# Performance work log

Measured on AMD Instinct MI355X. Metric: run time of the kernel, lower is better.

## Reference

```python
import jax, jax.numpy as jnp
import numpy as np

N_QUBITS = 6      # 4 data + 2 ancilla
N_DATA = 4
N_LAYERS = 4
N_GROUPS = 8
DIM = 2 ** N_QUBITS  # 64 statevector amplitudes (real: RY + CNOT keep state real)
GN_GROUPS = 32
EPS = 1e-5


def _cnot_ring_perm():
    # CNOT(q, q+1 mod n) ring applied sequentially; compose into one basis permutation.
    n = N_QUBITS
    f = np.arange(DIM)
    for c in range(n):
        t = (c + 1) % n
        cbit = (f >> (n - 1 - c)) & 1
        f = np.where(cbit == 1, f ^ (1 << (n - 1 - t)), f)
    # new_state[f[i]] = old_state[i]  =>  new = old[finv]
    finv = np.empty(DIM, dtype=np.int64)
    finv[f] = np.arange(DIM)
    return jnp.asarray(finv)


def _zsign():
    i = np.arange(DIM)[:, None]
    q = np.arange(N_DATA)[None, :]
    return jnp.asarray(1.0 - 2.0 * ((i >> (N_QUBITS - 1 - q)) & 1), dtype=jnp.float32)


PERM = _cnot_ring_perm()
ZSIGN = _zsign()


def _group_norm(x, gamma, beta):
    B, C, H, W = x.shape
    xg = x.reshape(B, GN_GROUPS, C // GN_GROUPS, H, W)
    mu = xg.mean(axis=(2, 3, 4), keepdims=True)
    var = xg.var(axis=(2, 3, 4), keepdims=True)
    xn = ((xg - mu) * jax.lax.rsqrt(var + EPS)).reshape(B, C, H, W)
    return xn * gamma[None, :, None, None] + beta[None, :, None, None]


def _apply_ry(state, half_angle, q):
    # state: [B,H,W,G,64]; half_angle: [B,H,W,G]; RY = [[c,-s],[s,c]] on qubit q
    pre, post = 2 ** q, 2 ** (N_QUBITS - 1 - q)
    s = state.reshape(state.shape[:-1] + (pre, 2, post))
    c = jnp.cos(half_angle)[..., None, None]
    sn = jnp.sin(half_angle)[..., None, None]
    a0, a1 = s[..., 0, :], s[..., 1, :]
    new = jnp.stack([c * a0 - sn * a1, sn * a0 + c * a1], axis=-2)
    return new.reshape(state.shape)


def _forward(x, emb, gamma, beta, w_in, b_in, theta, w_style, b_style, w_out, b_out):
    B, C, H, W = x.shape
    h = _group_norm(x, gamma, beta)                       # norm0
    emb_a = emb * jax.nn.sigmoid(emb)                     # SiLU(emb)
    # 1x1 projection to per-group data-qubit rotation angles: [B,H,W,G,4]
    ang = jnp.einsum('oc,bchw->bohw', w_in, h) + b_in[None, :, None, None]
    ang = ang.reshape(B, N_GROUPS, N_DATA, H, W).transpose(0, 3, 4, 1, 2)
    # style modulation of circuit parameters: [B,G,L,Q]
    style = (emb_a @ w_style.T + b_style).reshape(B, N_GROUPS, N_LAYERS, N_QUBITS)
    # init |0...0> per pixel per group
    state = jnp.zeros((B, H, W, N_GROUPS, DIM), x.dtype).at[..., 0].set(1.0)
    for l in range(N_LAYERS):
        for q in range(N_QUBITS):
            a = theta[:, l, q][None, None, None, :] + style[:, :, l, q][:, None, None, :]
            if q < N_DATA:                                # data reuploading each layer
                a = a + ang[..., q]
            state = _apply_ry(state, 0.5 * a, q)
        state = state[..., PERM]                          # CNOT ring entangler
    probs = state * state
    meas = probs @ ZSIGN                                  # [B,H,W,G,4] <Z> on data qubits
    meas = meas.transpose(0, 3, 4, 1, 2).reshape(B, N_GROUPS * N_DATA, H, W)
    out = jnp.einsum('oc,bchw->bohw', w_out, meas) + b_out[None, :, None, None]
    return out + x                                        # residual


def setup_inputs() -> dict:
    key = jax.random.key(0)
    ks = jax.random.split(key, 6)
    B, C, H, W, E = 16, 256, 32, 32, 512
    return {
        'x': jax.random.normal(ks[0], (B, C, H, W), jnp.float32),
        'emb': jax.random.normal(ks[1], (B, E), jnp.float32),
        'gamma': jnp.ones((C,), jnp.float32),
        'beta': jnp.zeros((C,), jnp.float32),
        'w_in': jax.random.normal(ks[2], (32, C), jnp.float32) * 0.1,
        'b_in': jnp.zeros((32,), jnp.float32),
        'theta': jax.random.normal(ks[3], (N_GROUPS, N_LAYERS, N_QUBITS), jnp.float32) * 0.5,
        'w_style': jax.random.normal(ks[4], (N_GROUPS * N_LAYERS * N_QUBITS, E), jnp.float32) * 0.02,
        'b_style': jnp.zeros((N_GROUPS * N_LAYERS * N_QUBITS,), jnp.float32),
        'w_out': jax.random.normal(ks[5], (C, 32), jnp.float32) * 0.05,
        'b_out': jnp.zeros((C,), jnp.float32),
    }


def reference(x, emb, gamma, beta, w_in, b_in, theta, w_style, b_style, w_out, b_out):
    return _forward(x, emb, gamma, beta, w_in, b_in, theta, w_style, b_style, w_out, b_out)
```

## Files before the change

kernel.cpp:

```cpp
#include <hip/hip_runtime.h>
#include <math.h>

#define NB 16
#define NC 256
#define NHW 1024
#define NE 512
#define NDQ 4
#define NLQ 4
#define NQB 6
#define QDIM 64
#define PIX 16
#define XPAD 260
#define MSP 20

typedef float v2f __attribute__((ext_vector_type(2)));

struct PermT { int v[QDIM]; };
constexpr PermT make_perm() {
    PermT P{};
    int f[QDIM] = {};
    for (int i = 0; i < QDIM; ++i) f[i] = i;
    for (int c = 0; c < NQB; ++c) {
        int t = (c + 1) % NQB;
        for (int i = 0; i < QDIM; ++i)
            if ((f[i] >> (NQB - 1 - c)) & 1) f[i] ^= 1 << (NQB - 1 - t);
    }
    for (int i = 0; i < QDIM; ++i) P.v[f[i]] = i;
    return P;
}
constexpr PermT PERM = make_perm();

#define ELEM(arr, j) (((j) & 1) ? arr[(j) >> 1].y : arr[(j) >> 1].x)

__global__ __launch_bounds__(256) void k_pre(const float* __restrict__ x,
                                             const float* __restrict__ emb,
                                             const float* __restrict__ w_style,
                                             const float* __restrict__ b_style,
                                             const float* __restrict__ theta,
                                             float* __restrict__ mu,
                                             float* __restrict__ rs,
                                             float* __restrict__ A) {
    if (blockIdx.x < 512) {
        int bg = blockIdx.x;
        const float4* xp = (const float4*)(x + (size_t)bg * 8 * NHW);
        float s = 0.f, ss = 0.f;
        for (int i = threadIdx.x; i < 8 * NHW / 4; i += 256) {
            float4 v = xp[i];
            s  += v.x + v.y + v.z + v.w;
            ss += v.x*v.x + v.y*v.y + v.z*v.z + v.w*v.w;
        }
        __shared__ float red0[4], red1[4];
        #pragma unroll
        for (int o = 32; o; o >>= 1) { s += __shfl_down(s, o); ss += __shfl_down(ss, o); }
        int lane = threadIdx.x & 63, w = threadIdx.x >> 6;
        if (lane == 0) { red0[w] = s; red1[w] = ss; }
        __syncthreads();
        if (threadIdx.x == 0) {
            s  = red0[0] + red0[1] + red0[2] + red0[3];
            ss = red1[0] + red1[1] + red1[2] + red1[3];
            float m = s * (1.f / 8192.f);
            float var = ss * (1.f / 8192.f) - m * m;
            mu[bg] = m;
            rs[bg] = rsqrtf(var + 1e-5f);
        }
    } else {
        int b = blockIdx.x - 512;
        __shared__ float es[NE];
        int t = threadIdx.x;
        for (int i = t; i < NE; i += 256) {
            float v = emb[b * NE + i];
            es[i] = v / (1.f + __expf(-v));
        }
        __syncthreads();
        int j0 = t >> 3, sub = t & 7;
        for (int pass = 0; pass < 6; ++pass) {
            int j = pass * 32 + j0;
            const float* wr = w_style + (size_t)j * NE + sub * 64;
            const float* er = es + sub * 64;
            float acc = 0.f;
            #pragma unroll
            for (int i = 0; i < 64; i += 4) {
                float4 w4 = *(const float4*)(wr + i);
                acc = fmaf(w4.x, er[i],   acc);
                acc = fmaf(w4.y, er[i+1], acc);
                acc = fmaf(w4.z, er[i+2], acc);
                acc = fmaf(w4.w, er[i+3], acc);
            }
            acc += __shfl_xor(acc, 1);
            acc += __shfl_xor(acc, 2);
            acc += __shfl_xor(acc, 4);
            if (sub == 0) A[b * 192 + j] = theta[j] + b_style[j] + acc;
        }
    }
}

__global__ __launch_bounds__(256, 4) void k_main(
    const float* __restrict__ x,
    const float* __restrict__ gamma,
    const float* __restrict__ beta,
    const float* __restrict__ w_in,
    const float* __restrict__ b_in,
    const float* __restrict__ A,
    const float* __restrict__ w_out,
    const float* __restrict__ b_out,
    const float* __restrict__ mu,
    const float* __restrict__ rs,
    float* __restrict__ out) {

    __shared__ float xs[PIX * XPAD];
    __shared__ float as_[PIX * 36];
    __shared__ float ms[32 * MSP];
    __shared__ float scs[NC], shs[NC];

    int blk = blockIdx.x;
    int b = blk >> 6;
    int pbase = (blk & 63) * PIX;
    int t = threadIdx.x;
    int c0 = t >> 2, f4 = (t & 3) * 4;

    float4 xr[4];
    #pragma unroll
    for (int k = 0; k < 4; ++k) {
        int c = c0 + 64 * k;
        xr[k] = *(const float4*)(x + (size_t)(b * NC + c) * NHW + pbase + f4);
    }
    {
        int g = b * 32 + (t >> 3);
        float r = rs[g], m = mu[g];
        float sc = r * gamma[t];
        scs[t] = sc;
        shs[t] = fmaf(-m, sc, beta[t]);
    }
    __syncthreads();

    #pragma unroll
    for (int k = 0; k < 4; ++k) {
        int c = c0 + 64 * k;
        float sc = scs[c], sh = shs[c];
        float4 v = xr[k];
        xs[(f4 + 0) * XPAD + c] = fmaf(v.x, sc, sh);
        xs[(f4 + 1) * XPAD + c] = fmaf(v.y, sc, sh);
        xs[(f4 + 2) * XPAD + c] = fmaf(v.z, sc, sh);
        xs[(f4 + 3) * XPAD + c] = fmaf(v.w, sc, sh);
    }
    __syncthreads();

    {
        int og2 = t >> 4, p = t & 15;
        int o0 = 2 * og2;
        const float* w0r = w_in + o0 * NC;
        const float* w1r = w_in + (o0 + 1) * NC;
        const float* hrow = xs + p * XPAD;
        float a0 = 0.f, a1 = 0.f;
        #pragma unroll 8
        for (int c = 0; c < NC; c += 4) {
            float4 h = *(const float4*)(hrow + c);
            float4 w0 = *(const float4*)(w0r + c);
            float4 w1 = *(const float4*)(w1r + c);
            a0 = fmaf(w0.x, h.x, fmaf(w0.y, h.y, fmaf(w0.z, h.z, fmaf(w0.w, h.w, a0))));
            a1 = fmaf(w1.x, h.x, fmaf(w1.y, h.y, fmaf(w1.z, h.z, fmaf(w1.w, h.w, a1))));
        }
        as_[p * 36 + o0]     = a0 + b_in[o0];
        as_[p * 36 + o0 + 1] = a1 + b_in[o0 + 1];
    }
    __syncthreads();

    #pragma unroll
    for (int k = 0; k < 4; ++k) {
        int c = c0 + 64 * k;
        float4 v = xr[k];
        xs[(f4 + 0) * XPAD + c] = v.x;
        xs[(f4 + 1) * XPAD + c] = v.y;
        xs[(f4 + 2) * XPAD + c] = v.z;
        xs[(f4 + 3) * XPAD + c] = v.w;
    }

    if (t < 128) {
        int g = t >> 4, p = t & 15;
        float4 angv = *(const float4*)(as_ + p * 36 + g * 4);
        float angp[NDQ] = {angv.x, angv.y, angv.z, angv.w};
        float Ar[24];
        {
            const float4* Ab4 = (const float4*)(A + b * 192 + g * 24);
            #pragma unroll
            for (int j = 0; j < 6; ++j) {
                float4 a4 = Ab4[j];
                Ar[4*j] = a4.x; Ar[4*j+1] = a4.y; Ar[4*j+2] = a4.z; Ar[4*j+3] = a4.w;
            }
        }

        v2f st2[QDIM / 2];
        #pragma unroll
        for (int k = 0; k < QDIM / 2; ++k) st2[k] = (v2f){0.f, 0.f};
        st2[0].x = 1.f;

        #pragma unroll
        for (int l = 0; l < NLQ; ++l) {
            #pragma unroll
            for (int q = 0; q < NQB; ++q) {
                float a = Ar[l * NQB + q] + (q < NDQ ? angp[q] : 0.f);
                float sn, cs;
                __sincosf(0.5f * a, &sn, &cs);
                v2f cs2 = {cs, cs};
                if (q < 5) {
                    const int m = 32 >> q;
                    v2f sn2 = {sn, sn};
                    #pragma unroll
                    for (int i = 0; i < QDIM; i += 2) {
                        if (i & m) continue;
                        int klo = i >> 1, khi = (i | m) >> 1;
                        v2f lo = st2[klo], hi = st2[khi];
                        v2f tm = sn2 * hi;
                        v2f um = cs2 * hi;
                        st2[klo] = __builtin_elementwise_fma(cs2, lo, -tm);
                        st2[khi] = __builtin_elementwise_fma(sn2, lo, um);
                    }
                } else {
                    v2f msn = {-sn, sn};
                    #pragma unroll
                    for (int k = 0; k < QDIM / 2; ++k) {
                        v2f a0 = st2[k];
                        v2f asw = __builtin_shufflevector(a0, a0, 1, 0);
                        st2[k] = __builtin_elementwise_fma(msn, asw, cs2 * a0);
                    }
                }
            }
            v2f nst[QDIM / 2];
            #pragma unroll
            for (int k = 0; k < QDIM / 2; ++k) {
                v2f n;
                n.x = ELEM(st2, PERM.v[2 * k]);
                n.y = ELEM(st2, PERM.v[2 * k + 1]);
                nst[k] = n;
            }
            #pragma unroll
            for (int k = 0; k < QDIM / 2; ++k) st2[k] = nst[k];
        }

        float s4[16];
        #pragma unroll
        for (int h = 0; h < 16; ++h) {
            v2f p0 = st2[2 * h] * st2[2 * h];
            v2f p1 = st2[2 * h + 1] * st2[2 * h + 1];
            s4[h] = (p0.x + p0.y) + (p1.x + p1.y);
        }
        float meas[NDQ] = {0.f, 0.f, 0.f, 0.f};
        #pragma unroll
        for (int h = 0; h < 16; ++h) {
            #pragma unroll
            for (int d = 0; d < NDQ; ++d) {
                if ((h >> (3 - d)) & 1) meas[d] -= s4[h];
                else                    meas[d] += s4[h];
            }
        }
        #pragma unroll
        for (int d = 0; d < NDQ; ++d) ms[(g * 4 + d) * MSP + p] = meas[d];
    }
    __syncthreads();

    {
        int c2 = t >> 3, f2 = (t & 7) * 2;
        v2f mreg[32];
        #pragma unroll
        for (int o = 0; o < 32; ++o)
            mreg[o] = *(const v2f*)(ms + o * MSP + f2);
        #pragma unroll
        for (int k = 0; k < 8; ++k) {
            int c = c2 + 32 * k;
            const float* wr = w_out + c * 32;
            float ax = 0.f, ay = 0.f;
            #pragma unroll
            for (int o = 0; o < 32; o += 4) {
                float4 w4 = *(const float4*)(wr + o);
                v2f m0 = mreg[o], m1 = mreg[o+1], m2 = mreg[o+2], m3 = mreg[o+3];
                ax = fmaf(w4.x, m0.x, fmaf(w4.y, m1.x, fmaf(w4.z, m2.x, fmaf(w4.w, m3.x, ax))));
                ay = fmaf(w4.x, m0.y, fmaf(w4.y, m1.y, fmaf(w4.z, m2.y, fmaf(w4.w, m3.y, ay))));
            }
            float bo = b_out[c];
            float x0 = xs[(f2 + 0) * XPAD + c];
            float x1 = xs[(f2 + 1) * XPAD + c];
            float2 r = {ax + bo + x0, ay + bo + x1};
            *(float2*)(out + (size_t)(b * NC + c) * NHW + pbase + f2) = r;
        }
    }
}

extern "C" void kernel_launch(void* const* d_in, const int* in_sizes, int n_in,
                              void* d_out, int out_size, void* d_ws, size_t ws_size,
                              hipStream_t stream) {
    const float* x       = (const float*)d_in[0];
    const float* emb     = (const float*)d_in[1];
    const float* gamma   = (const float*)d_in[2];
    const float* beta    = (const float*)d_in[3];
    const float* w_in    = (const float*)d_in[4];
    const float* b_in    = (const float*)d_in[5];
    const float* theta   = (const float*)d_in[6];
    const float* w_style = (const float*)d_in[7];
    const float* b_style = (const float*)d_in[8];
    const float* w_out   = (const float*)d_in[9];
    const float* b_out   = (const float*)d_in[10];
    float* out = (float*)d_out;

    float* ws = (float*)d_ws;
    float* mu = ws;
    float* rs = ws + 512;
    float* A  = ws + 1024;

    k_pre<<<512 + NB, 256, 0, stream>>>(x, emb, w_style, b_style, theta, mu, rs, A);
    k_main<<<NB * 64, 256, 0, stream>>>(x, gamma, beta, w_in, b_in, A,
                                        w_out, b_out, mu, rs, out);
}
```

Measured before the change: 138.5 us.

## Fuse GroupNorm stats and style projection into main kernel with per-batch spin barrier

Removes the separate pre-pass kernel. Each main block now accumulates GroupNorm sums from the x tile it already loads, and computes part of the style projection, both through global atomics. The 64 blocks of a batch then synchronise on a global counter, with a timeout fallback that recomputes the stats locally. This avoids a second full read of x and one kernel launch, at the cost of a memset, atomics, and a spin barrier that assumes all 64 blocks of a batch are co-resident. With a grid of 1024 blocks at 4 blocks per CU, co-residency should hold on this GPU.

```diff
diff --git a/kernel.cpp b/kernel.cpp
--- a/kernel.cpp
+++ b/kernel.cpp
@@ -32,91 +32,43 @@
 
 #define ELEM(arr, j) (((j) & 1) ? arr[(j) >> 1].y : arr[(j) >> 1].x)
 
-__global__ __launch_bounds__(256) void k_pre(const float* __restrict__ x,
-                                             const float* __restrict__ emb,
-                                             const float* __restrict__ w_style,
-                                             const float* __restrict__ b_style,
-                                             const float* __restrict__ theta,
-                                             float* __restrict__ mu,
-                                             float* __restrict__ rs,
-                                             float* __restrict__ A) {
-    if (blockIdx.x < 512) {
-        int bg = blockIdx.x;
-        const float4* xp = (const float4*)(x + (size_t)bg * 8 * NHW);
-        float s = 0.f, ss = 0.f;
-        for (int i = threadIdx.x; i < 8 * NHW / 4; i += 256) {
-            float4 v = xp[i];
-            s  += v.x + v.y + v.z + v.w;
-            ss += v.x*v.x + v.y*v.y + v.z*v.z + v.w*v.w;
-        }
-        __shared__ float red0[4], red1[4];
-        #pragma unroll
-        for (int o = 32; o; o >>= 1) { s += __shfl_down(s, o); ss += __shfl_down(ss, o); }
-        int lane = threadIdx.x & 63, w = threadIdx.x >> 6;
-        if (lane == 0) { red0[w] = s; red1[w] = ss; }
-        __syncthreads();
-        if (threadIdx.x == 0) {
-            s  = red0[0] + red0[1] + red0[2] + red0[3];
-            ss = red1[0] + red1[1] + red1[2] + red1[3];
-            float m = s * (1.f / 8192.f);
-            float var = ss * (1.f / 8192.f) - m * m;
-            mu[bg] = m;
-            rs[bg] = rsqrtf(var + 1e-5f);
-        }
-    } else {
-        int b = blockIdx.x - 512;
-        __shared__ float es[NE];
-        int t = threadIdx.x;
-        for (int i = t; i < NE; i += 256) {
-            float v = emb[b * NE + i];
-            es[i] = v / (1.f + __expf(-v));
-        }
-        __syncthreads();
-        int j0 = t >> 3, sub = t & 7;
-        for (int pass = 0; pass < 6; ++pass) {
-            int j = pass * 32 + j0;
-            const float* wr = w_style + (size_t)j * NE + sub * 64;
-            const float* er = es + sub * 64;
-            float acc = 0.f;
-            #pragma unroll
-            for (int i = 0; i < 64; i += 4) {
-                float4 w4 = *(const float4*)(wr + i);
-                acc = fmaf(w4.x, er[i],   acc);
-                acc = fmaf(w4.y, er[i+1], acc);
-                acc = fmaf(w4.z, er[i+2], acc);
-                acc = fmaf(w4.w, er[i+3], acc);
-            }
-            acc += __shfl_xor(acc, 1);
-            acc += __shfl_xor(acc, 2);
-            acc += __shfl_xor(acc, 4);
-            if (sub == 0) A[b * 192 + j] = theta[j] + b_style[j] + acc;
-        }
-    }
-}
-
-__global__ __launch_bounds__(256, 4) void k_main(
+#define WS_DONE 1024
+#define WS_A    1056
+#define WS_ZERO_BYTES ((WS_A + 192 * NB) * 4)
+
+__global__ __launch_bounds__(256, 4) void k_mega(
     const float* __restrict__ x,
+    const float* __restrict__ emb,
     const float* __restrict__ gamma,
     const float* __restrict__ beta,
     const float* __restrict__ w_in,
     const float* __restrict__ b_in,
-    const float* __restrict__ A,
+    const float* __restrict__ theta,
+    const float* __restrict__ w_style,
+    const float* __restrict__ b_style,
     const float* __restrict__ w_out,
     const float* __restrict__ b_out,
-    const float* __restrict__ mu,
-    const float* __restrict__ rs,
+    float* __restrict__ ws,
     float* __restrict__ out) {
 
     __shared__ float xs[PIX * XPAD];
     __shared__ float as_[PIX * 36];
     __shared__ float ms[32 * MSP];
-    __shared__ float scs[NC], shs[NC];
+    __shared__ float mure[32], rsre[32];
+    __shared__ float Als[192];
+    __shared__ int s_timeout;
+
+    float* stats_s  = ws;
+    float* stats_ss = ws + 512;
+    unsigned* doneu = (unsigned*)(ws + WS_DONE);
+    float* Ag       = ws + WS_A;
 
     int blk = blockIdx.x;
     int b = blk >> 6;
     int pbase = (blk & 63) * PIX;
     int t = threadIdx.x;
     int c0 = t >> 2, f4 = (t & 3) * 4;
+    int wv = t >> 6;
 
     float4 xr[4];
     #pragma unroll
@@ -124,19 +76,105 @@
         int c = c0 + 64 * k;
         xr[k] = *(const float4*)(x + (size_t)(b * NC + c) * NHW + pbase + f4);
     }
-    {
-        int g = b * 32 + (t >> 3);
-        float r = rs[g], m = mu[g];
-        float sc = r * gamma[t];
-        scs[t] = sc;
-        shs[t] = fmaf(-m, sc, beta[t]);
+
+    #pragma unroll
+    for (int k = 0; k < 4; ++k) {
+        float4 v = xr[k];
+        float s  = v.x + v.y + v.z + v.w;
+        float ss = v.x*v.x + v.y*v.y + v.z*v.z + v.w*v.w;
+        #pragma unroll
+        for (int o = 1; o < 32; o <<= 1) { s += __shfl_xor(s, o); ss += __shfl_xor(ss, o); }
+        if ((t & 31) == 0) {
+            int g = (c0 >> 3) + 8 * k;
+            atomicAdd(&stats_s[b * 32 + g], s);
+            atomicAdd(&stats_ss[b * 32 + g], ss);
+        }
+    }
+
+    if (wv >= 1) {
+        int j = (blk & 63) * 3 + (wv - 1);
+        int lane = t & 63;
+        const float4* er = (const float4*)(emb + (size_t)b * NE + lane * 8);
+        const float4* wr = (const float4*)(w_style + (size_t)j * NE + lane * 8);
+        float acc = 0.f;
+        #pragma unroll
+        for (int i = 0; i < 2; ++i) {
+            float4 e4 = er[i], w4 = wr[i];
+            float s0 = e4.x / (1.f + __expf(-e4.x));
+            float s1 = e4.y / (1.f + __expf(-e4.y));
+            float s2 = e4.z / (1.f + __expf(-e4.z));
+            float s3 = e4.w / (1.f + __expf(-e4.w));
+            acc = fmaf(w4.x, s0, fmaf(w4.y, s1, fmaf(w4.z, s2, fmaf(w4.w, s3, acc))));
+        }
+        #pragma unroll
+        for (int o = 1; o < 64; o <<= 1) acc += __shfl_xor(acc, o);
+        if (lane == 0) atomicAdd(&Ag[b * 192 + j], acc + theta[j] + b_style[j]);
+    }
+
+    __syncthreads();
+    if (t == 0) {
+        __threadfence();
+        atomicAdd(&doneu[b], 1u);
+        int spins = 0, to = 0;
+        while (atomicAdd(&doneu[b], 0u) < 64u) {
+            if (++spins > 60000) { to = 1; break; }
+            __builtin_amdgcn_s_sleep(8);
+        }
+        s_timeout = to;
+    }
+    __syncthreads();
+    __threadfence();
+
+    if (!s_timeout) {
+        if (t < 32) {
+            float s  = atomicAdd(&stats_s[b * 32 + t], 0.0f);
+            float ss = atomicAdd(&stats_ss[b * 32 + t], 0.0f);
+            float m = s * (1.f / 8192.f);
+            mure[t] = m;
+            rsre[t] = rsqrtf(ss * (1.f / 8192.f) - m * m + 1e-5f);
+        }
+        if (t < 192) Als[t] = atomicAdd(&Ag[b * 192 + t], 0.0f);
+    } else {
+        {
+            const float4* row = (const float4*)(x + (size_t)(b * NC + t) * NHW);
+            float s = 0.f, ss = 0.f;
+            for (int i = 0; i < 256; ++i) {
+                float4 v = row[i];
+                s  += v.x + v.y + v.z + v.w;
+                ss += v.x*v.x + v.y*v.y + v.z*v.z + v.w*v.w;
+            }
+            #pragma unroll
+            for (int o = 1; o < 8; o <<= 1) { s += __shfl_xor(s, o); ss += __shfl_xor(ss, o); }
+            if ((t & 7) == 0) {
+                int g = t >> 3;
+                float m = s * (1.f / 8192.f);
+                mure[g] = m;
+                rsre[g] = rsqrtf(ss * (1.f / 8192.f) - m * m + 1e-5f);
+            }
+        }
+        if (t < 192) {
+            const float4* er = (const float4*)(emb + (size_t)b * NE);
+            const float4* wr = (const float4*)(w_style + (size_t)t * NE);
+            float acc = 0.f;
+            for (int i = 0; i < 128; ++i) {
+                float4 e4 = er[i], w4 = wr[i];
+                float s0 = e4.x / (1.f + __expf(-e4.x));
+                float s1 = e4.y / (1.f + __expf(-e4.y));
+                float s2 = e4.z / (1.f + __expf(-e4.z));
+                float s3 = e4.w / (1.f + __expf(-e4.w));
+                acc = fmaf(w4.x, s0, fmaf(w4.y, s1, fmaf(w4.z, s2, fmaf(w4.w, s3, acc))));
+            }
+            Als[t] = acc + theta[t] + b_style[t];
+        }
     }
     __syncthreads();
 
     #pragma unroll
     for (int k = 0; k < 4; ++k) {
         int c = c0 + 64 * k;
-        float sc = scs[c], sh = shs[c];
+        int g = c >> 3;
+        float sc = rsre[g] * gamma[c];
+        float sh = fmaf(-mure[g], sc, beta[c]);
         float4 v = xr[k];
         xs[(f4 + 0) * XPAD + c] = fmaf(v.x, sc, sh);
         xs[(f4 + 1) * XPAD + c] = fmaf(v.y, sc, sh);
@@ -179,15 +217,7 @@
         int g = t >> 4, p = t & 15;
         float4 angv = *(const float4*)(as_ + p * 36 + g * 4);
         float angp[NDQ] = {angv.x, angv.y, angv.z, angv.w};
-        float Ar[24];
-        {
-            const float4* Ab4 = (const float4*)(A + b * 192 + g * 24);
-            #pragma unroll
-            for (int j = 0; j < 6; ++j) {
-                float4 a4 = Ab4[j];
-                Ar[4*j] = a4.x; Ar[4*j+1] = a4.y; Ar[4*j+2] = a4.z; Ar[4*j+3] = a4.w;
-            }
-        }
+        const float* Ab = Als + g * 24;
 
         v2f st2[QDIM / 2];
         #pragma unroll
@@ -198,7 +228,7 @@
         for (int l = 0; l < NLQ; ++l) {
             #pragma unroll
             for (int q = 0; q < NQB; ++q) {
-                float a = Ar[l * NQB + q] + (q < NDQ ? angp[q] : 0.f);
+                float a = Ab[l * NQB + q] + (q < NDQ ? angp[q] : 0.f);
                 float sn, cs;
                 __sincosf(0.5f * a, &sn, &cs);
                 v2f cs2 = {cs, cs};
@@ -300,13 +330,10 @@
     const float* w_out   = (const float*)d_in[9];
     const float* b_out   = (const float*)d_in[10];
     float* out = (float*)d_out;
-
     float* ws = (float*)d_ws;
-    float* mu = ws;
-    float* rs = ws + 512;
-    float* A  = ws + 1024;
-
-    k_pre<<<512 + NB, 256, 0, stream>>>(x, emb, w_style, b_style, theta, mu, rs, A);
-    k_main<<<NB * 64, 256, 0, stream>>>(x, gamma, beta, w_in, b_in, A,
-                                        w_out, b_out, mu, rs, out);
+
+    hipMemsetAsync(ws, 0, WS_ZERO_BYTES, stream);
+
+    k_mega<<<NB * 64, 256, 0, stream>>>(x, emb, gamma, beta, w_in, b_in, theta,
+                                        w_style, b_style, w_out, b_out, ws, out);
 }
```

Result: slower. 286.8 us (+107.1%).

## Halve main kernel block size and give each thread more work

Applied to the files above, without the earlier changes.

The main kernel now runs with 128 threads instead of 256. Each thread loads 8 channel vectors, computes 4 projection outputs and writes 16 output channels. Before, half the threads sat idle during the quantum-circuit phase; now every thread runs that phase. The group-norm scale and shift are computed inline from global memory rather than through a shared-memory staging step, which removes one barrier. In exchange, each thread holds more registers, which may lower occupancy, and per-thread serial work grows in the projection and output phases.

```diff
diff --git a/kernel.cpp b/kernel.cpp
--- a/kernel.cpp
+++ b/kernel.cpp
@@ -94,7 +94,7 @@
     }
 }
 
-__global__ __launch_bounds__(256, 4) void k_main(
+__global__ __launch_bounds__(128, 4) void k_main(
     const float* __restrict__ x,
     const float* __restrict__ gamma,
     const float* __restrict__ beta,
@@ -110,7 +110,6 @@
     __shared__ float xs[PIX * XPAD];
     __shared__ float as_[PIX * 36];
     __shared__ float ms[32 * MSP];
-    __shared__ float scs[NC], shs[NC];
 
     int blk = blockIdx.x;
     int b = blk >> 6;
@@ -118,25 +117,19 @@
     int t = threadIdx.x;
     int c0 = t >> 2, f4 = (t & 3) * 4;
 
-    float4 xr[4];
+    float4 xr[8];
     #pragma unroll
-    for (int k = 0; k < 4; ++k) {
-        int c = c0 + 64 * k;
+    for (int k = 0; k < 8; ++k) {
+        int c = c0 + 32 * k;
         xr[k] = *(const float4*)(x + (size_t)(b * NC + c) * NHW + pbase + f4);
     }
-    {
-        int g = b * 32 + (t >> 3);
-        float r = rs[g], m = mu[g];
-        float sc = r * gamma[t];
-        scs[t] = sc;
-        shs[t] = fmaf(-m, sc, beta[t]);
-    }
-    __syncthreads();
 
     #pragma unroll
-    for (int k = 0; k < 4; ++k) {
-        int c = c0 + 64 * k;
-        float sc = scs[c], sh = shs[c];
+    for (int k = 0; k < 8; ++k) {
+        int c = c0 + 32 * k;
+        int g = b * 32 + (c >> 3);
+        float sc = rs[g] * gamma[c];
+        float sh = fmaf(-mu[g], sc, beta[c]);
         float4 v = xr[k];
         xs[(f4 + 0) * XPAD + c] = fmaf(v.x, sc, sh);
         xs[(f4 + 1) * XPAD + c] = fmaf(v.y, sc, sh);
@@ -146,28 +139,32 @@
     __syncthreads();
 
     {
-        int og2 = t >> 4, p = t & 15;
-        int o0 = 2 * og2;
-        const float* w0r = w_in + o0 * NC;
-        const float* w1r = w_in + (o0 + 1) * NC;
+        int og = t >> 4, p = t & 15;
+        int o0 = og * 4;
+        const float* wbase = w_in + o0 * NC;
         const float* hrow = xs + p * XPAD;
-        float a0 = 0.f, a1 = 0.f;
+        float a0 = 0.f, a1 = 0.f, a2 = 0.f, a3 = 0.f;
         #pragma unroll 8
         for (int c = 0; c < NC; c += 4) {
             float4 h = *(const float4*)(hrow + c);
-            float4 w0 = *(const float4*)(w0r + c);
-            float4 w1 = *(const float4*)(w1r + c);
+            float4 w0 = *(const float4*)(wbase + c);
+            float4 w1 = *(const float4*)(wbase + NC + c);
+            float4 w2 = *(const float4*)(wbase + 2 * NC + c);
+            float4 w3 = *(const float4*)(wbase + 3 * NC + c);
             a0 = fmaf(w0.x, h.x, fmaf(w0.y, h.y, fmaf(w0.z, h.z, fmaf(w0.w, h.w, a0))));
             a1 = fmaf(w1.x, h.x, fmaf(w1.y, h.y, fmaf(w1.z, h.z, fmaf(w1.w, h.w, a1))));
-        }
-        as_[p * 36 + o0]     = a0 + b_in[o0];
-        as_[p * 36 + o0 + 1] = a1 + b_in[o0 + 1];
+            a2 = fmaf(w2.x, h.x, fmaf(w2.y, h.y, fmaf(w2.z, h.z, fmaf(w2.w, h.w, a2))));
+            a3 = fmaf(w3.x, h.x, fmaf(w3.y, h.y, fmaf(w3.z, h.z, fmaf(w3.w, h.w, a3))));
+        }
+        float4 bi = *(const float4*)(b_in + o0);
+        float4 r = {a0 + bi.x, a1 + bi.y, a2 + bi.z, a3 + bi.w};
+        *(float4*)(as_ + p * 36 + o0) = r;
     }
     __syncthreads();
 
     #pragma unroll
-    for (int k = 0; k < 4; ++k) {
-        int c = c0 + 64 * k;
+    for (int k = 0; k < 8; ++k) {
+        int c = c0 + 32 * k;
         float4 v = xr[k];
         xs[(f4 + 0) * XPAD + c] = v.x;
         xs[(f4 + 1) * XPAD + c] = v.y;
@@ -175,7 +172,7 @@
         xs[(f4 + 3) * XPAD + c] = v.w;
     }
 
-    if (t < 128) {
+    {
         int g = t >> 4, p = t & 15;
         float4 angv = *(const float4*)(as_ + p * 36 + g * 4);
         float angp[NDQ] = {angv.x, angv.y, angv.z, angv.w};
@@ -265,8 +262,8 @@
         for (int o = 0; o < 32; ++o)
             mreg[o] = *(const v2f*)(ms + o * MSP + f2);
         #pragma unroll
-        for (int k = 0; k < 8; ++k) {
-            int c = c2 + 32 * k;
+        for (int k = 0; k < 16; ++k) {
+            int c = c2 + 16 * k;
             const float* wr = w_out + c * 32;
             float ax = 0.f, ay = 0.f;
             #pragma unroll
@@ -307,6 +304,6 @@
     float* A  = ws + 1024;
 
     k_pre<<<512 + NB, 256, 0, stream>>>(x, emb, w_style, b_style, theta, mu, rs, A);
-    k_main<<<NB * 64, 256, 0, stream>>>(x, gamma, beta, w_in, b_in, A,
+    k_main<<<NB * 64, 128, 0, stream>>>(x, gamma, beta, w_in, b_in, A,
                                         w_out, b_out, mu, rs, out);
 }
```

Result: slower. 161.2 us (+16.4%).

## Split each circuit statevector across two lanes and fold CNOT permutations into gate indexing

Applied to the files above, without the earlier changes.

Each 64-amplitude circuit simulation is split across two threads of 32 amplitudes each. The qubit held across the lane pair is handled with shfl_xor exchanges. The per-layer CNOT ring permutation is removed by working in a permuted basis, where each gate's partner index and sign pattern come from constexpr tables. The block shrinks to 128 threads and 8 pixels so all threads run the circuit, with packed-FMA rewrites of the projections and the shared scale/shift staging dropped. This targets the idle half-block and the register pressure of the old 64-amplitude circuit loop, at the cost of extra shuffles and a smaller per-block tile.

```diff
diff --git a/kernel.cpp b/kernel.cpp
--- a/kernel.cpp
+++ b/kernel.cpp
@@ -9,28 +9,42 @@
 #define NLQ 4
 #define NQB 6
 #define QDIM 64
-#define PIX 16
+#define PIX 8
 #define XPAD 260
-#define MSP 20
+#define MSP 12
 
 typedef float v2f __attribute__((ext_vector_type(2)));
 
-struct PermT { int v[QDIM]; };
-constexpr PermT make_perm() {
-    PermT P{};
-    int f[QDIM] = {};
-    for (int i = 0; i < QDIM; ++i) f[i] = i;
+constexpr int fwd1(int i) {
+    int r = i;
     for (int c = 0; c < NQB; ++c) {
         int t = (c + 1) % NQB;
-        for (int i = 0; i < QDIM; ++i)
-            if ((f[i] >> (NQB - 1 - c)) & 1) f[i] ^= 1 << (NQB - 1 - t);
-    }
-    for (int i = 0; i < QDIM; ++i) P.v[f[i]] = i;
-    return P;
-}
-constexpr PermT PERM = make_perm();
-
-#define ELEM(arr, j) (((j) & 1) ? arr[(j) >> 1].y : arr[(j) >> 1].x)
+        if ((r >> (NQB - 1 - c)) & 1) r ^= 1 << (NQB - 1 - t);
+    }
+    return r;
+}
+constexpr int fwdl(int s, int l) { for (int i = 0; i < l; ++i) s = fwd1(s); return s; }
+constexpr int parity6(int x) { x ^= x >> 4; x ^= x >> 2; x ^= x >> 1; return x & 1; }
+
+struct GateTab { int M[NLQ][NQB]; int V[NLQ][NQB]; int W[NDQ]; };
+constexpr GateTab make_tab() {
+    GateTab g{};
+    for (int l = 0; l < NLQ; ++l)
+        for (int q = 0; q < NQB; ++q) {
+            int m = 1 << (NQB - 1 - q);
+            for (int x = 0; x < QDIM; ++x) if (fwdl(x, l) == m) { g.M[l][q] = x; break; }
+            int V = 0;
+            for (int t = 0; t < NQB; ++t) V |= ((fwdl(1 << t, l) >> (NQB - 1 - q)) & 1) << t;
+            g.V[l][q] = V;
+        }
+    for (int d = 0; d < NDQ; ++d) {
+        int W = 0;
+        for (int t = 0; t < NQB; ++t) W |= ((fwdl(1 << t, NLQ) >> (NQB - 1 - d)) & 1) << t;
+        g.W[d] = W;
+    }
+    return g;
+}
+constexpr GateTab GT = make_tab();
 
 __global__ __launch_bounds__(256) void k_pre(const float* __restrict__ x,
                                              const float* __restrict__ emb,
@@ -94,7 +108,7 @@
     }
 }
 
-__global__ __launch_bounds__(256, 4) void k_main(
+__global__ __launch_bounds__(128, 2) void k_main(
     const float* __restrict__ x,
     const float* __restrict__ gamma,
     const float* __restrict__ beta,
@@ -110,13 +124,12 @@
     __shared__ float xs[PIX * XPAD];
     __shared__ float as_[PIX * 36];
     __shared__ float ms[32 * MSP];
-    __shared__ float scs[NC], shs[NC];
 
     int blk = blockIdx.x;
-    int b = blk >> 6;
-    int pbase = (blk & 63) * PIX;
+    int b = blk >> 7;
+    int pbase = (blk & 127) * PIX;
     int t = threadIdx.x;
-    int c0 = t >> 2, f4 = (t & 3) * 4;
+    int c0 = t >> 1, f4 = (t & 1) * 4;
 
     float4 xr[4];
     #pragma unroll
@@ -124,19 +137,13 @@
         int c = c0 + 64 * k;
         xr[k] = *(const float4*)(x + (size_t)(b * NC + c) * NHW + pbase + f4);
     }
-    {
-        int g = b * 32 + (t >> 3);
-        float r = rs[g], m = mu[g];
-        float sc = r * gamma[t];
-        scs[t] = sc;
-        shs[t] = fmaf(-m, sc, beta[t]);
-    }
-    __syncthreads();
 
     #pragma unroll
     for (int k = 0; k < 4; ++k) {
         int c = c0 + 64 * k;
-        float sc = scs[c], sh = shs[c];
+        int g = b * 32 + (c >> 3);
+        float sc = rs[g] * gamma[c];
+        float sh = fmaf(-mu[g], sc, beta[c]);
         float4 v = xr[k];
         xs[(f4 + 0) * XPAD + c] = fmaf(v.x, sc, sh);
         xs[(f4 + 1) * XPAD + c] = fmaf(v.y, sc, sh);
@@ -146,22 +153,20 @@
     __syncthreads();
 
     {
-        int og2 = t >> 4, p = t & 15;
-        int o0 = 2 * og2;
-        const float* w0r = w_in + o0 * NC;
-        const float* w1r = w_in + (o0 + 1) * NC;
-        const float* hrow = xs + p * XPAD;
-        float a0 = 0.f, a1 = 0.f;
-        #pragma unroll 8
-        for (int c = 0; c < NC; c += 4) {
-            float4 h = *(const float4*)(hrow + c);
-            float4 w0 = *(const float4*)(w0r + c);
-            float4 w1 = *(const float4*)(w1r + c);
-            a0 = fmaf(w0.x, h.x, fmaf(w0.y, h.y, fmaf(w0.z, h.z, fmaf(w0.w, h.w, a0))));
-            a1 = fmaf(w1.x, h.x, fmaf(w1.y, h.y, fmaf(w1.z, h.z, fmaf(w1.w, h.w, a1))));
-        }
-        as_[p * 36 + o0]     = a0 + b_in[o0];
-        as_[p * 36 + o0 + 1] = a1 + b_in[o0 + 1];
+        int og = t >> 3, p = t & 7;
+        int o0 = og * 2;
+        const v2f* h2  = (const v2f*)(xs + p * XPAD);
+        const v2f* w02 = (const v2f*)(w_in + o0 * NC);
+        const v2f* w12 = (const v2f*)(w_in + (o0 + 1) * NC);
+        v2f a0 = {0.f, 0.f}, a1 = {0.f, 0.f};
+        #pragma unroll 16
+        for (int c2 = 0; c2 < NC / 2; ++c2) {
+            v2f h = h2[c2];
+            a0 = __builtin_elementwise_fma(w02[c2], h, a0);
+            a1 = __builtin_elementwise_fma(w12[c2], h, a1);
+        }
+        as_[p * 36 + o0]     = a0.x + a0.y + b_in[o0];
+        as_[p * 36 + o0 + 1] = a1.x + a1.y + b_in[o0 + 1];
     }
     __syncthreads();
 
@@ -175,8 +180,9 @@
         xs[(f4 + 3) * XPAD + c] = v.w;
     }
 
-    if (t < 128) {
-        int g = t >> 4, p = t & 15;
+    {
+        int cir = t >> 1, sub = t & 1;
+        int g = cir >> 3, p = cir & 7;
         float4 angv = *(const float4*)(as_ + p * 36 + g * 4);
         float angp[NDQ] = {angv.x, angv.y, angv.z, angv.w};
         float Ar[24];
@@ -189,97 +195,98 @@
             }
         }
 
-        v2f st2[QDIM / 2];
-        #pragma unroll
-        for (int k = 0; k < QDIM / 2; ++k) st2[k] = (v2f){0.f, 0.f};
-        st2[0].x = 1.f;
+        v2f st2[16];
+        #pragma unroll
+        for (int k = 0; k < 16; ++k) st2[k] = (v2f){0.f, 0.f};
+        if (sub == 0) st2[0].x = 1.f;
 
         #pragma unroll
         for (int l = 0; l < NLQ; ++l) {
             #pragma unroll
             for (int q = 0; q < NQB; ++q) {
+                const int M  = GT.M[l][q];
+                const int V  = GT.V[l][q];
+                const int ML = M & 31;
+                const int KD = ML >> 1;
                 float a = Ar[l * NQB + q] + (q < NDQ ? angp[q] : 0.f);
                 float sn, cs;
                 __sincosf(0.5f * a, &sn, &cs);
+                float snS = (V & 32) ? (sub ? -sn : sn) : sn;
                 v2f cs2 = {cs, cs};
-                if (q < 5) {
-                    const int m = 32 >> q;
-                    v2f sn2 = {sn, sn};
+                if (M & 32) {
+                    v2f pstl[16];
                     #pragma unroll
-                    for (int i = 0; i < QDIM; i += 2) {
-                        if (i & m) continue;
-                        int klo = i >> 1, khi = (i | m) >> 1;
-                        v2f lo = st2[klo], hi = st2[khi];
-                        v2f tm = sn2 * hi;
-                        v2f um = cs2 * hi;
-                        st2[klo] = __builtin_elementwise_fma(cs2, lo, -tm);
-                        st2[khi] = __builtin_elementwise_fma(sn2, lo, um);
+                    for (int k = 0; k < 16; ++k) {
+                        pstl[k].x = __shfl_xor(st2[k].x, 1);
+                        pstl[k].y = __shfl_xor(st2[k].y, 1);
+                    }
+                    #pragma unroll
+                    for (int k = 0; k < 16; ++k) {
+                        v2f ov = pstl[k ^ KD];
+                        if (M & 1) ov = __builtin_shufflevector(ov, ov, 1, 0);
+                        v2f co = { parity6((2*k)     & (V & 31)) ? snS : -snS,
+                                   parity6((2*k + 1) & (V & 31)) ? snS : -snS };
+                        st2[k] = __builtin_elementwise_fma(co, ov, cs2 * st2[k]);
                     }
                 } else {
-                    v2f msn = {-sn, sn};
+                    v2f nst[16];
                     #pragma unroll
-                    for (int k = 0; k < QDIM / 2; ++k) {
-                        v2f a0 = st2[k];
-                        v2f asw = __builtin_shufflevector(a0, a0, 1, 0);
-                        st2[k] = __builtin_elementwise_fma(msn, asw, cs2 * a0);
+                    for (int k = 0; k < 16; ++k) {
+                        v2f ov = st2[k ^ KD];
+                        if (M & 1) ov = __builtin_shufflevector(ov, ov, 1, 0);
+                        v2f co = { parity6((2*k)     & (V & 31)) ? snS : -snS,
+                                   parity6((2*k + 1) & (V & 31)) ? snS : -snS };
+                        nst[k] = __builtin_elementwise_fma(co, ov, cs2 * st2[k]);
                     }
+                    #pragma unroll
+                    for (int k = 0; k < 16; ++k) st2[k] = nst[k];
                 }
             }
-            v2f nst[QDIM / 2];
-            #pragma unroll
-            for (int k = 0; k < QDIM / 2; ++k) {
-                v2f n;
-                n.x = ELEM(st2, PERM.v[2 * k]);
-                n.y = ELEM(st2, PERM.v[2 * k + 1]);
-                nst[k] = n;
-            }
-            #pragma unroll
-            for (int k = 0; k < QDIM / 2; ++k) st2[k] = nst[k];
-        }
-
-        float s4[16];
-        #pragma unroll
-        for (int h = 0; h < 16; ++h) {
-            v2f p0 = st2[2 * h] * st2[2 * h];
-            v2f p1 = st2[2 * h + 1] * st2[2 * h + 1];
-            s4[h] = (p0.x + p0.y) + (p1.x + p1.y);
-        }
-        float meas[NDQ] = {0.f, 0.f, 0.f, 0.f};
-        #pragma unroll
-        for (int h = 0; h < 16; ++h) {
-            #pragma unroll
-            for (int d = 0; d < NDQ; ++d) {
-                if ((h >> (3 - d)) & 1) meas[d] -= s4[h];
-                else                    meas[d] += s4[h];
-            }
-        }
-        #pragma unroll
-        for (int d = 0; d < NDQ; ++d) ms[(g * 4 + d) * MSP + p] = meas[d];
+        }
+
+        #pragma unroll
+        for (int k = 0; k < 16; ++k) st2[k] = st2[k] * st2[k];
+        #pragma unroll
+        for (int d = 0; d < NDQ; ++d) {
+            const int W = GT.W[d];
+            v2f acc2 = {0.f, 0.f};
+            #pragma unroll
+            for (int k = 0; k < 16; ++k) {
+                v2f sg = { parity6((2*k)     & (W & 31)) ? -1.f : 1.f,
+                           parity6((2*k + 1) & (W & 31)) ? -1.f : 1.f };
+                acc2 = __builtin_elementwise_fma(sg, st2[k], acc2);
+            }
+            float pd = acc2.x + acc2.y;
+            if (W & 32) pd = sub ? -pd : pd;
+            pd += __shfl_xor(pd, 1);
+            if (sub == 0) ms[(g * 4 + d) * MSP + p] = pd;
+        }
     }
     __syncthreads();
 
     {
-        int c2 = t >> 3, f2 = (t & 7) * 2;
+        int cb = t >> 2, f2 = (t & 3) * 2;
         v2f mreg[32];
         #pragma unroll
         for (int o = 0; o < 32; ++o)
             mreg[o] = *(const v2f*)(ms + o * MSP + f2);
         #pragma unroll
         for (int k = 0; k < 8; ++k) {
-            int c = c2 + 32 * k;
+            int c = cb + 32 * k;
             const float* wr = w_out + c * 32;
-            float ax = 0.f, ay = 0.f;
-            #pragma unroll
-            for (int o = 0; o < 32; o += 4) {
-                float4 w4 = *(const float4*)(wr + o);
-                v2f m0 = mreg[o], m1 = mreg[o+1], m2 = mreg[o+2], m3 = mreg[o+3];
-                ax = fmaf(w4.x, m0.x, fmaf(w4.y, m1.x, fmaf(w4.z, m2.x, fmaf(w4.w, m3.x, ax))));
-                ay = fmaf(w4.x, m0.y, fmaf(w4.y, m1.y, fmaf(w4.z, m2.y, fmaf(w4.w, m3.y, ay))));
+            v2f acc = {0.f, 0.f};
+            #pragma unroll
+            for (int o4 = 0; o4 < 8; ++o4) {
+                float4 w4 = *(const float4*)(wr + o4 * 4);
+                acc = __builtin_elementwise_fma((v2f){w4.x, w4.x}, mreg[4*o4],     acc);
+                acc = __builtin_elementwise_fma((v2f){w4.y, w4.y}, mreg[4*o4 + 1], acc);
+                acc = __builtin_elementwise_fma((v2f){w4.z, w4.z}, mreg[4*o4 + 2], acc);
+                acc = __builtin_elementwise_fma((v2f){w4.w, w4.w}, mreg[4*o4 + 3], acc);
             }
             float bo = b_out[c];
             float x0 = xs[(f2 + 0) * XPAD + c];
             float x1 = xs[(f2 + 1) * XPAD + c];
-            float2 r = {ax + bo + x0, ay + bo + x1};
+            float2 r = {acc.x + bo + x0, acc.y + bo + x1};
             *(float2*)(out + (size_t)(b * NC + c) * NHW + pbase + f2) = r;
         }
     }
@@ -307,6 +314,6 @@
     float* A  = ws + 1024;
 
     k_pre<<<512 + NB, 256, 0, stream>>>(x, emb, w_style, b_style, theta, mu, rs, A);
-    k_main<<<NB * 64, 256, 0, stream>>>(x, gamma, beta, w_in, b_in, A,
-                                        w_out, b_out, mu, rs, out);
-}
+    k_main<<<NB * 128, 128, 0, stream>>>(x, gamma, beta, w_in, b_in, A,
+                                         w_out, b_out, mu, rs, out);
+}
```

Result: no change. 141.1 us (+1.8%).
